# Optimization experiments

Hardware: AMD Instinct MI355X
Metric: run time of the kernel (lower is better)

## Reference

```python
import jax, jax.numpy as jnp
import numpy as np

N = 50000   # nodes
E = 800000  # edges
IN, HID, HEADS, OUT = 128, 32, 4, 64
NEG_SLOPE = 0.2


def _gatv2_layer(x, src, dst, Wl, bl, Wr, br, att, bias, res_W, concat):
    """One PyG-style GATv2Conv layer (eval mode, no dropout).
    x: [N, F_in]; att: [H, C]. Returns [N, H*C] if concat else [N, C]."""
    H, C = att.shape
    xl = (x @ Wl + bl).reshape(N, H, C)   # source transform
    xr = (x @ Wr + br).reshape(N, H, C)   # target transform
    e = jax.nn.leaky_relu(xl[src] + xr[dst], NEG_SLOPE)        # [E, H, C]
    logit = jnp.einsum('ehc,hc->eh', e, att)                   # [E, H]
    # segment softmax over incoming edges per destination node
    m = jax.ops.segment_max(logit, dst, num_segments=N)        # [N, H]
    p = jnp.exp(logit - m[dst])
    denom = jax.ops.segment_sum(p, dst, num_segments=N)
    alpha = p / (denom[dst] + 1e-16)                           # [E, H]
    out = jax.ops.segment_sum(xl[src] * alpha[:, :, None], dst, num_segments=N)  # [N, H, C]
    out = out.reshape(N, H * C) if concat else out.mean(axis=1)
    if res_W is not None:
        out = out + x @ res_W
    return out + bias


def _glorot(key, shape):
    fan_in = shape[0] if len(shape) > 1 else shape[-1]
    return jax.random.normal(key, shape, dtype=jnp.float32) / np.sqrt(fan_in)


def setup_inputs() -> dict:
    key = jax.random.key(0)
    ks = iter(jax.random.split(key, 32))
    x = jax.random.normal(next(ks), (N, IN), dtype=jnp.float32)
    edge_index = jax.random.randint(next(ks), (2, E), 0, N, dtype=jnp.int64)
    d = {"x": x, "edge_index": edge_index}
    HC = HEADS * HID  # 128
    # layer 0: IN -> HEADS*HID, concat, residual
    d["Wl0"] = _glorot(next(ks), (IN, HC)); d["bl0"] = jnp.zeros((HC,), jnp.float32)
    d["Wr0"] = _glorot(next(ks), (IN, HC)); d["br0"] = jnp.zeros((HC,), jnp.float32)
    d["att0"] = _glorot(next(ks), (HEADS, HID)); d["b0"] = jnp.zeros((HC,), jnp.float32)
    d["res0"] = _glorot(next(ks), (IN, HC))
    # layer 1: HC -> HEADS*HID, concat, residual
    d["Wl1"] = _glorot(next(ks), (HC, HC)); d["bl1"] = jnp.zeros((HC,), jnp.float32)
    d["Wr1"] = _glorot(next(ks), (HC, HC)); d["br1"] = jnp.zeros((HC,), jnp.float32)
    d["att1"] = _glorot(next(ks), (HEADS, HID)); d["b1"] = jnp.zeros((HC,), jnp.float32)
    d["res1"] = _glorot(next(ks), (HC, HC))
    # layer 2: HC -> OUT, heads=1, concat=False, no residual
    d["Wl2"] = _glorot(next(ks), (HC, OUT)); d["bl2"] = jnp.zeros((OUT,), jnp.float32)
    d["Wr2"] = _glorot(next(ks), (HC, OUT)); d["br2"] = jnp.zeros((OUT,), jnp.float32)
    d["att2"] = _glorot(next(ks), (1, OUT)); d["b2"] = jnp.zeros((OUT,), jnp.float32)
    return d


def reference(x, edge_index,
              Wl0, bl0, Wr0, br0, att0, b0, res0,
              Wl1, bl1, Wr1, br1, att1, b1, res1,
              Wl2, bl2, Wr2, br2, att2, b2):
    src, dst = edge_index[0], edge_index[1]
    h = _gatv2_layer(x, src, dst, Wl0, bl0, Wr0, br0, att0, b0, res0, True)
    h = jax.nn.elu(h)
    h = _gatv2_layer(h, src, dst, Wl1, bl1, Wr1, br1, att1, b1, res1, True)
    h = jax.nn.elu(h)
    return _gatv2_layer(h, src, dst, Wl2, bl2, Wr2, br2, att2, b2, None, False)
```

## Files before the change

### kernel.cpp

```cpp
#include <hip/hip_runtime.h>
#include <math.h>

#define NN 50000
#define EE 800000
#define NBK 196
#define EPB 4096

typedef short v8s __attribute__((ext_vector_type(8)));
typedef float v4f __attribute__((ext_vector_type(4)));

__device__ __forceinline__ ushort f2bf(float f) {
    uint u = __float_as_uint(f);
    uint r = (u + 0x7fffu + ((u >> 16) & 1u)) >> 16;
    return (ushort)r;
}
__device__ __forceinline__ float bf2f(ushort h) {
    return __uint_as_float(((uint)h) << 16);
}
__device__ __forceinline__ float lrelu(float x) {
    return fmaf(0.4f, fabsf(x), 0.6f * x);
}

template <int CTRL>
__device__ __forceinline__ float dppadd(float x) {
    int y = __builtin_amdgcn_update_dpp(0, __float_as_int(x), CTRL, 0xf, 0xf, true);
    return x + __int_as_float(y);
}
__device__ __forceinline__ float sum8(float x) {
    x = dppadd<0xB1>(x);
    x = dppadd<0x4E>(x);
    x = dppadd<0x141>(x);
    return x;
}
__device__ __forceinline__ float sum16(float x) {
    x = sum8(x);
    x = dppadd<0x140>(x);
    return x;
}
__device__ __forceinline__ float expclamp(float t) {
    return __expf(fminf(fmaxf(t, -60.f), 80.f));
}

__global__ __launch_bounds__(256) void k_bktcnt(const int* __restrict__ edst,
                                                int* __restrict__ bcnt) {
    __shared__ int h[NBK];
    int t = threadIdx.x;
    if (t < NBK) h[t] = 0;
    __syncthreads();
    int eb = blockIdx.x * EPB;
    #pragma unroll
    for (int k = 0; k < EPB / 256; ++k) {
        int e = eb + k * 256 + t;
        if (e < EE) atomicAdd(&h[edst[e] >> 8], 1);
    }
    __syncthreads();
    if (t < NBK && h[t]) atomicAdd(&bcnt[t], h[t]);
}

__global__ __launch_bounds__(256) void k_bscan(const int* __restrict__ bcnt,
                                               int* __restrict__ bbase,
                                               int* __restrict__ bcur) {
    __shared__ int sm[256];
    int t = threadIdx.x;
    int v = (t < NBK) ? bcnt[t] : 0;
    sm[t] = v;
    __syncthreads();
    for (int o = 1; o < 256; o <<= 1) {
        int a = (t >= o) ? sm[t - o] : 0;
        __syncthreads();
        sm[t] += a;
        __syncthreads();
    }
    if (t < NBK) { int ex = sm[t] - v; bbase[t] = ex; bcur[t] = ex; }
}

__global__ __launch_bounds__(256) void k_bktplace(const int* __restrict__ esrc,
                                                  const int* __restrict__ edst,
                                                  int* __restrict__ bcur,
                                                  uint* __restrict__ ebuf) {
    __shared__ int h[NBK];
    __shared__ int base[NBK];
    int t = threadIdx.x;
    if (t < NBK) h[t] = 0;
    __syncthreads();
    int eb = blockIdx.x * EPB;
    int pk[EPB / 256];
    #pragma unroll
    for (int k = 0; k < EPB / 256; ++k) {
        int e = eb + k * 256 + t;
        pk[k] = -1;
        if (e < EE) {
            int b = edst[e] >> 8;
            int r = atomicAdd(&h[b], 1);
            pk[k] = (b << 16) | r;
        }
    }
    __syncthreads();
    if (t < NBK && h[t]) base[t] = atomicAdd(&bcur[t], h[t]);
    __syncthreads();
    #pragma unroll
    for (int k = 0; k < EPB / 256; ++k) {
        int e = eb + k * 256 + t;
        if (e < EE) {
            int b = pk[k] >> 16;
            int r = pk[k] & 0xFFFF;
            uint dl = (uint)(edst[e] & 255);
            ebuf[base[b] + r] = (dl << 16) | (uint)esrc[e];
        }
    }
}

__global__ __launch_bounds__(256) void k_bktfin(const uint* __restrict__ ebuf,
                                                const int* __restrict__ bbase,
                                                const int* __restrict__ bcnt,
                                                int* __restrict__ rowptr,
                                                int* __restrict__ csrc) {
    __shared__ int deg[256];
    __shared__ int sm[256];
    __shared__ int cur[256];
    const int b = blockIdx.x;
    const int t = threadIdx.x;
    const int eb = bbase[b];
    const int ec = bcnt[b];
    deg[t] = 0;
    __syncthreads();
    for (int k = t; k < ec; k += 256)
        atomicAdd(&deg[ebuf[eb + k] >> 16], 1);
    __syncthreads();
    int v = deg[t];
    sm[t] = v;
    __syncthreads();
    for (int o = 1; o < 256; o <<= 1) {
        int a = (t >= o) ? sm[t - o] : 0;
        __syncthreads();
        sm[t] += a;
        __syncthreads();
    }
    int node = b * 256 + t;
    if (node < NN) rowptr[node + 1] = eb + sm[t];
    if (node == 0) rowptr[0] = 0;
    cur[t] = sm[t] - v;
    __syncthreads();
    for (int k = t; k < ec; k += 256) {
        uint u = ebuf[eb + k];
        int nl = (int)(u >> 16);
        int r = atomicAdd(&cur[nl], 1);
        csrc[eb + r] = (int)(u & 0xFFFFu);
    }
}

struct WPack {
    const float* W[8];
    ushort* Th[8];
    ushort* Tl[8];
    int fout[8];
};

__global__ __launch_bounds__(256) void k_conv_w(WPack p) {
    int wi = blockIdx.y;
    int fout = p.fout[wi];
    int total = 128 * fout;
    int i = blockIdx.x * 256 + threadIdx.x;
    if (i >= total) return;
    int k = i / fout;
    int n = i - k * fout;
    float f = p.W[wi][i];
    ushort h = f2bf(f);
    float lo = f - bf2f(h);
    int t = n >> 4, m = n & 15, c = k >> 5, quad = (k >> 3) & 3, j = k & 7;
    int flat = ((((t * 4 + c) * 4 + quad) * 16 + m) << 3) + j;
    p.Th[wi][flat] = h;
    p.Tl[wi][flat] = f2bf(lo);
}

template <int FOUT, int NMAT, bool CVT>
__global__ __launch_bounds__(256) void k_gemm_fused(
    const float* __restrict__ Xf,
    const ushort* __restrict__ Xh, const ushort* __restrict__ Xl,
    const ushort* __restrict__ T0h, const ushort* __restrict__ T0l, const float* __restrict__ B0,
    const ushort* __restrict__ T1h, const ushort* __restrict__ T1l, const float* __restrict__ B1,
    const ushort* __restrict__ T2h, const ushort* __restrict__ T2l,
    const float* __restrict__ ATT, float* __restrict__ DR,
    ushort* __restrict__ O0b, float* __restrict__ O1, float* __restrict__ O2)
{
    constexpr int NH  = (FOUT == 128) ? 4 : 1;
    constexpr int RS  = FOUT + ((FOUT == 128) ? 8 : 4);
    constexpr int NT  = FOUT / 16;
    constexpr int TPH = NT / NH;

    const int lane = threadIdx.x & 63;
    const int wid  = threadIdx.x >> 6;
    const int m    = lane & 15;
    const int quad = lane >> 4;
    const int row0 = blockIdx.x * 64 + wid * 16;

    v8s ah[4], al[4];
    {
        int arow = row0 + m;
        if (arow > NN - 1) arow = NN - 1;
        #pragma unroll
        for (int c = 0; c < 4; ++c) {
            size_t off = (size_t)arow * 128 + c * 32 + quad * 8;
            if constexpr (CVT) {
                float4 f0 = *(const float4*)(Xf + off);
                float4 f1 = *(const float4*)(Xf + off + 4);
                const float fe[8] = {f0.x, f0.y, f0.z, f0.w, f1.x, f1.y, f1.z, f1.w};
                #pragma unroll
                for (int e = 0; e < 8; ++e) {
                    ushort h = f2bf(fe[e]);
                    float lo = fe[e] - bf2f(h);
                    ah[c][e] = (short)h;
                    al[c][e] = (short)(__float_as_uint(lo) >> 16);
                }
            } else {
                ah[c] = *(const v8s*)(Xh + off);
                al[c] = *(const v8s*)(Xl + off);
            }
        }
    }

    float dp0[4] = {0.f, 0.f, 0.f, 0.f};
    float dp1[4] = {0.f, 0.f, 0.f, 0.f};

    #pragma unroll
    for (int t = 0; t < NT; ++t) {
        v4f a0 = {0.f, 0.f, 0.f, 0.f};
        v4f a1 = {0.f, 0.f, 0.f, 0.f};
        v4f a2 = {0.f, 0.f, 0.f, 0.f};
        #pragma unroll
        for (int c = 0; c < 4; ++c) {
            const int boff = t * 2048 + (c * 4 + quad) * 128 + m * 8;
            v8s b0h = *(const v8s*)(T0h + boff);
            v8s b0l = *(const v8s*)(T0l + boff);
            v8s b1h = *(const v8s*)(T1h + boff);
            v8s b1l = *(const v8s*)(T1l + boff);
            a0 = __builtin_amdgcn_mfma_f32_16x16x32_bf16(al[c], b0h, a0, 0, 0, 0);
            a1 = __builtin_amdgcn_mfma_f32_16x16x32_bf16(al[c], b1h, a1, 0, 0, 0);
            a0 = __builtin_amdgcn_mfma_f32_16x16x32_bf16(ah[c], b0l, a0, 0, 0, 0);
            a1 = __builtin_amdgcn_mfma_f32_16x16x32_bf16(ah[c], b1l, a1, 0, 0, 0);
            a0 = __builtin_amdgcn_mfma_f32_16x16x32_bf16(ah[c], b0h, a0, 0, 0, 0);
            a1 = __builtin_amdgcn_mfma_f32_16x16x32_bf16(ah[c], b1h, a1, 0, 0, 0);
            if constexpr (NMAT == 3) {
                v8s b2h = *(const v8s*)(T2h + boff);
                v8s b2l = *(const v8s*)(T2l + boff);
                a2 = __builtin_amdgcn_mfma_f32_16x16x32_bf16(al[c], b2h, a2, 0, 0, 0);
                a2 = __builtin_amdgcn_mfma_f32_16x16x32_bf16(ah[c], b2l, a2, 0, 0, 0);
                a2 = __builtin_amdgcn_mfma_f32_16x16x32_bf16(ah[c], b2h, a2, 0, 0, 0);
            }
        }
        const int col = t * 16 + m;
        const float bad0 = B0[col];
        const float bad1 = B1[col];
        const float attc = ATT[col];
        #pragma unroll
        for (int j = 0; j < 4; ++j) {
            float o0v = a0[j] + bad0;
            float o1v = a1[j] + bad1;
            dp0[j] = fmaf(attc, o0v, dp0[j]);
            dp1[j] = fmaf(attc, o1v, dp1[j]);
            int r = row0 + quad * 4 + j;
            if (r < NN) {
                O0b[(size_t)r * RS + col] = f2bf(o0v);
                O1[(size_t)r * FOUT + col] = o1v;
                if constexpr (NMAT == 3) O2[(size_t)r * FOUT + col] = a2[j];
            }
        }
        if ((t % TPH) == TPH - 1) {
            const int h = t / TPH;
            #pragma unroll
            for (int j = 0; j < 4; ++j) {
                float s0 = sum16(dp0[j]);
                float s1 = sum16(dp1[j]);
                int r = row0 + quad * 4 + j;
                if (m == 0 && r < NN) {
                    *(float*)(O0b + (size_t)r * RS + FOUT + 2 * h) = 0.6f * s0;
                    DR[(size_t)r * NH + h] = 0.6f * s1;
                }
                dp0[j] = 0.f;
                dp1[j] = 0.f;
            }
        }
    }
}

__global__ __launch_bounds__(256) void k_agg01(const ushort* __restrict__ XLb,
                                               const float4* __restrict__ XR4,
                                               const float4* __restrict__ RES4,
                                               const float* __restrict__ att,
                                               const float* __restrict__ bias,
                                               const float* __restrict__ DR,
                                               const int* __restrict__ rowptr,
                                               const int* __restrict__ csrc,
                                               ushort* __restrict__ Hh,
                                               ushort* __restrict__ Hl) {
    const int lane = threadIdx.x & 63;
    const int wid = threadIdx.x >> 6;
    const int n = blockIdx.x * 4 + wid;
    if (n >= NN) return;
    const int beg = rowptr[n];
    const int end = rowptr[n + 1];
    const int half = lane >> 5;
    const uint j = lane & 31;
    const int head = (int)(j >> 3);

    const float4 xr = XR4[(uint)n * 32u + j];
    float4 at = ((const float4*)att)[j];
    at.x *= 0.4f; at.y *= 0.4f; at.z *= 0.4f; at.w *= 0.4f;
    const float dRn = DR[(uint)n * 4u + (uint)head];
    float4 s = {0.f, 0.f, 0.f, 0.f};
    float d = 0.f;

#define EDGE01(U, DL)  {                                              \
    float4 v = {bf2f((U).x), bf2f((U).y), bf2f((U).z), bf2f((U).w)};  \
    float t0 =      at.x * fabsf(v.x + xr.x);                         \
    t0 = fmaf(at.y, fabsf(v.y + xr.y), t0);                           \
    t0 = fmaf(at.z, fabsf(v.z + xr.z), t0);                           \
    t0 = fmaf(at.w, fabsf(v.w + xr.w), t0);                           \
    float p = expclamp(sum8(t0) + (DL) + dRn);                        \
    d += p;                                                            \
    s.x = fmaf(p, v.x, s.x); s.y = fmaf(p, v.y, s.y);                 \
    s.z = fmaf(p, v.z, s.z); s.w = fmaf(p, v.w, s.w); }

    int i = beg;
    for (; i + 8 <= end; i += 8) {
        uint sa = (uint)csrc[i + half];
        uint sb = (uint)csrc[i + 2 + half];
        uint sc = (uint)csrc[i + 4 + half];
        uint sd = (uint)csrc[i + 6 + half];
        const ushort* pa = XLb + (size_t)sa * 136u;
        const ushort* pb = XLb + (size_t)sb * 136u;
        const ushort* pc = XLb + (size_t)sc * 136u;
        const ushort* pd = XLb + (size_t)sd * 136u;
        ushort4 ua = *(const ushort4*)(pa + 4u * j);
        float  da_ = *(const float*)(pa + 128 + 2 * head);
        ushort4 ub = *(const ushort4*)(pb + 4u * j);
        float  db_ = *(const float*)(pb + 128 + 2 * head);
        ushort4 uc = *(const ushort4*)(pc + 4u * j);
        float  dc_ = *(const float*)(pc + 128 + 2 * head);
        ushort4 ud = *(const ushort4*)(pd + 4u * j);
        float  dd_ = *(const float*)(pd + 128 + 2 * head);
        EDGE01(ua, da_)
        EDGE01(ub, db_)
        EDGE01(uc, dc_)
        EDGE01(ud, dd_)
    }
    for (; i < end; i += 2) {
        int ia = i + half;
        if (ia > end - 1) ia = end - 1;
        uint sa = (uint)csrc[ia];
        const ushort* pa = XLb + (size_t)sa * 136u;
        ushort4 ua = *(const ushort4*)(pa + 4u * j);
        float  da_ = *(const float*)(pa + 128 + 2 * head);
        float4 v = {bf2f(ua.x), bf2f(ua.y), bf2f(ua.z), bf2f(ua.w)};
        float t0 =      at.x * fabsf(v.x + xr.x);
        t0 = fmaf(at.y, fabsf(v.y + xr.y), t0);
        t0 = fmaf(at.z, fabsf(v.z + xr.z), t0);
        t0 = fmaf(at.w, fabsf(v.w + xr.w), t0);
        float p = expclamp(sum8(t0) + da_ + dRn);
        if (half && (i + 1 >= end)) p = 0.f;
        d += p;
        s.x = fmaf(p, v.x, s.x); s.y = fmaf(p, v.y, s.y);
        s.z = fmaf(p, v.z, s.z); s.w = fmaf(p, v.w, s.w);
    }
#undef EDGE01

    d   += __shfl_xor(d, 32);
    s.x += __shfl_xor(s.x, 32);
    s.y += __shfl_xor(s.y, 32);
    s.z += __shfl_xor(s.z, 32);
    s.w += __shfl_xor(s.w, 32);

    if (half == 0) {
        float inv = (d > 0.f) ? 1.f / d : 0.f;
        float4 rv = RES4[(uint)n * 32u + j];
        float4 bv = ((const float4*)bias)[j];
        float o0 = fmaf(s.x, inv, rv.x + bv.x);
        float o1 = fmaf(s.y, inv, rv.y + bv.y);
        float o2 = fmaf(s.z, inv, rv.z + bv.z);
        float o3 = fmaf(s.w, inv, rv.w + bv.w);
        o0 = o0 > 0.f ? o0 : __expf(o0) - 1.f;
        o1 = o1 > 0.f ? o1 : __expf(o1) - 1.f;
        o2 = o2 > 0.f ? o2 : __expf(o2) - 1.f;
        o3 = o3 > 0.f ? o3 : __expf(o3) - 1.f;
        ushort4 h, l;
        h.x = f2bf(o0); l.x = f2bf(o0 - bf2f(h.x));
        h.y = f2bf(o1); l.y = f2bf(o1 - bf2f(h.y));
        h.z = f2bf(o2); l.z = f2bf(o2 - bf2f(h.z));
        h.w = f2bf(o3); l.w = f2bf(o3 - bf2f(h.w));
        *(ushort4*)(Hh + (uint)n * 128u + 4u * j) = h;
        *(ushort4*)(Hl + (uint)n * 128u + 4u * j) = l;
    }
}

__global__ __launch_bounds__(256) void k_agg2(const ushort* __restrict__ XLb,
                                              const float4* __restrict__ XR4,
                                              const float* __restrict__ att,
                                              const float* __restrict__ bias,
                                              const float* __restrict__ DR,
                                              const int* __restrict__ rowptr,
                                              const int* __restrict__ csrc,
                                              float* __restrict__ OUT) {
    const int lane = threadIdx.x & 63;
    const int wid = threadIdx.x >> 6;
    const int n = blockIdx.x * 4 + wid;
    if (n >= NN) return;
    const int beg = rowptr[n];
    const int end = rowptr[n + 1];
    const int q = lane >> 4;
    const uint jj = lane & 15;

    const float4 xr = XR4[(uint)n * 16u + jj];
    float4 at = ((const float4*)att)[jj];
    at.x *= 0.4f; at.y *= 0.4f; at.z *= 0.4f; at.w *= 0.4f;
    const float dRn = DR[n];
    float4 s = {0.f, 0.f, 0.f, 0.f};
    float d = 0.f;
    const int e1 = end - 1;

    for (int i = beg; i < end; i += 8) {
        int i0 = i + q;
        int i1 = i + 4 + q;
        uint s0 = (uint)csrc[min(i0, e1)];
        uint s1 = (uint)csrc[min(i1, e1)];
        const ushort* p0 = XLb + (size_t)s0 * 68u;
        const ushort* p1 = XLb + (size_t)s1 * 68u;
        ushort4 u0 = *(const ushort4*)(p0 + 4u * jj);
        float  dl0 = *(const float*)(p0 + 64);
        ushort4 u1 = *(const ushort4*)(p1 + 4u * jj);
        float  dl1 = *(const float*)(p1 + 64);
        #pragma unroll
        for (int u = 0; u < 2; ++u) {
            ushort4 uv = (u == 0) ? u0 : u1;
            float  dlv = (u == 0) ? dl0 : dl1;
            int ii = (u == 0) ? i0 : i1;
            float4 v = {bf2f(uv.x), bf2f(uv.y), bf2f(uv.z), bf2f(uv.w)};
            float t0 =      at.x * fabsf(v.x + xr.x);
            t0 = fmaf(at.y, fabsf(v.y + xr.y), t0);
            t0 = fmaf(at.z, fabsf(v.z + xr.z), t0);
            t0 = fmaf(at.w, fabsf(v.w + xr.w), t0);
            float p = expclamp(sum16(t0) + dlv + dRn);
            if (ii >= end) p = 0.f;
            d += p;
            s.x = fmaf(p, v.x, s.x); s.y = fmaf(p, v.y, s.y);
            s.z = fmaf(p, v.z, s.z); s.w = fmaf(p, v.w, s.w);
        }
    }

    d   += __shfl_xor(d, 16);   d   += __shfl_xor(d, 32);
    s.x += __shfl_xor(s.x, 16); s.x += __shfl_xor(s.x, 32);
    s.y += __shfl_xor(s.y, 16); s.y += __shfl_xor(s.y, 32);
    s.z += __shfl_xor(s.z, 16); s.z += __shfl_xor(s.z, 32);
    s.w += __shfl_xor(s.w, 16); s.w += __shfl_xor(s.w, 32);

    if (lane < 16) {
        float inv = (d > 0.f) ? 1.f / d : 0.f;
        float4 bv = ((const float4*)bias)[jj];
        float4 o;
        o.x = fmaf(s.x, inv, bv.x);
        o.y = fmaf(s.y, inv, bv.y);
        o.z = fmaf(s.z, inv, bv.z);
        o.w = fmaf(s.w, inv, bv.w);
        *(float4*)(OUT + (uint)n * 64u + 4u * jj) = o;
    }
}

extern "C" void kernel_launch(void* const* d_in, const int* in_sizes, int n_in,
                              void* d_out, int out_size, void* d_ws, size_t ws_size,
                              hipStream_t stream) {
    const float* x    = (const float*)d_in[0];
    const int*   ei   = (const int*)d_in[1];
    const int*   esrc = ei;
    const int*   edst = ei + EE;

    const float* Wl0 = (const float*)d_in[2];
    const float* bl0 = (const float*)d_in[3];
    const float* Wr0 = (const float*)d_in[4];
    const float* br0 = (const float*)d_in[5];
    const float* at0 = (const float*)d_in[6];
    const float* b0  = (const float*)d_in[7];
    const float* rs0 = (const float*)d_in[8];
    const float* Wl1 = (const float*)d_in[9];
    const float* bl1 = (const float*)d_in[10];
    const float* Wr1 = (const float*)d_in[11];
    const float* br1 = (const float*)d_in[12];
    const float* at1 = (const float*)d_in[13];
    const float* b1  = (const float*)d_in[14];
    const float* rs1 = (const float*)d_in[15];
    const float* Wl2 = (const float*)d_in[16];
    const float* bl2 = (const float*)d_in[17];
    const float* Wr2 = (const float*)d_in[18];
    const float* br2 = (const float*)d_in[19];
    const float* at2 = (const float*)d_in[20];
    const float* b2  = (const float*)d_in[21];

    float* out = (float*)d_out;

    ushort* XLb = (ushort*)d_ws;
    float* XR  = (float*)(XLb + (size_t)NN * 136);
    float* RES = XR + (size_t)NN * 128;
    ushort* Xh = (ushort*)(RES + (size_t)NN * 128);
    ushort* Xl_ = Xh + (size_t)NN * 128;
    float* DRarr = (float*)(Xl_ + (size_t)NN * 128);
    ushort* Wth = (ushort*)(DRarr + (size_t)NN * 4);
    const int wsz[8] = {16384, 16384, 16384, 16384, 16384, 16384, 8192, 8192};
    ushort* th[8]; ushort* tl[8];
    {
        ushort* p = Wth;
        for (int i = 0; i < 8; ++i) { th[i] = p; p += wsz[i]; }
        for (int i = 0; i < 8; ++i) { tl[i] = p; p += wsz[i]; }
    }
    int* bcnt   = (int*)(Wth + 2 * (6 * 16384 + 2 * 8192));
    int* bbase  = bcnt + 256;
    int* bcur   = bbase + 256;
    int* rowptr = bcur + 256;
    int* csrc   = rowptr + (NN + 1);
    uint* ebuf  = (uint*)(csrc + EE);

    hipMemsetAsync(bcnt, 0, 256 * sizeof(int), stream);
    const int ebk = (EE + EPB - 1) / EPB;
    k_bktcnt<<<ebk, 256, 0, stream>>>(edst, bcnt);
    k_bscan<<<1, 256, 0, stream>>>(bcnt, bbase, bcur);
    k_bktplace<<<ebk, 256, 0, stream>>>(esrc, edst, bcur, ebuf);
    k_bktfin<<<NBK, 256, 0, stream>>>(ebuf, bbase, bcnt, rowptr, csrc);

    WPack wp;
    const float* Ws[8] = {Wl0, Wr0, rs0, Wl1, Wr1, rs1, Wl2, Wr2};
    const int fouts[8] = {128, 128, 128, 128, 128, 128, 64, 64};
    for (int i = 0; i < 8; ++i) { wp.W[i] = Ws[i]; wp.Th[i] = th[i]; wp.Tl[i] = tl[i]; wp.fout[i] = fouts[i]; }
    k_conv_w<<<dim3(64, 8), 256, 0, stream>>>(wp);

    const int gemm_gx = (NN + 63) / 64;
    const int agg_grid = (NN + 3) / 4;

    k_gemm_fused<128, 3, true><<<gemm_gx, 256, 0, stream>>>(x, nullptr, nullptr,
        th[0], tl[0], bl0, th[1], tl[1], br0, th[2], tl[2], at0, DRarr, XLb, XR, RES);
    k_agg01<<<agg_grid, 256, 0, stream>>>(XLb, (const float4*)XR, (const float4*)RES,
        at0, b0, DRarr, rowptr, csrc, Xh, Xl_);

    k_gemm_fused<128, 3, false><<<gemm_gx, 256, 0, stream>>>(nullptr, Xh, Xl_,
        th[3], tl[3], bl1, th[4], tl[4], br1, th[5], tl[5], at1, DRarr, XLb, XR, RES);
    k_agg01<<<agg_grid, 256, 0, stream>>>(XLb, (const float4*)XR, (const float4*)RES,
        at1, b1, DRarr, rowptr, csrc, Xh, Xl_);

    k_gemm_fused<64, 2, false><<<gemm_gx, 256, 0, stream>>>(nullptr, Xh, Xl_,
        th[6], tl[6], bl2, th[7], tl[7], br2, nullptr, nullptr, at2, DRarr, XLb, XR, nullptr);
    k_agg2<<<agg_grid, 256, 0, stream>>>(XLb, (const float4*)XR, at2, b2, DRarr, rowptr, csrc, out);
}
```

Baseline: 365.5 us.

## Split GEMM output tiles across grid y and move per-node attention dots to separate arrays

The fused GEMM kernel now covers only two 16-column tiles per block, with blockIdx.y choosing the slice. This gives four times (or twice, for the last layer) as many blocks, raising parallelism at the cost of reloading and converting the A rows once per slice. The source-side attention dot products move out of the padded 136/68-stride bf16 rows into a separate DL array, so XLb becomes densely packed. In the last layer the per-node dots are summed with atomics across the two column slices, which needs two extra memsets. The aggregation kernels read DL through a separate gather, adding one scattered load per edge.

```diff
diff --git a/kernel.cpp b/kernel.cpp
--- a/kernel.cpp
+++ b/kernel.cpp
@@ -173,26 +173,22 @@
     p.Tl[wi][flat] = f2bf(lo);
 }
 
-template <int FOUT, int NMAT, bool CVT>
+template <int FOUT, int NMAT, bool CVT, int TS>
 __global__ __launch_bounds__(256) void k_gemm_fused(
     const float* __restrict__ Xf,
     const ushort* __restrict__ Xh, const ushort* __restrict__ Xl,
     const ushort* __restrict__ T0h, const ushort* __restrict__ T0l, const float* __restrict__ B0,
     const ushort* __restrict__ T1h, const ushort* __restrict__ T1l, const float* __restrict__ B1,
     const ushort* __restrict__ T2h, const ushort* __restrict__ T2l,
-    const float* __restrict__ ATT, float* __restrict__ DR,
+    const float* __restrict__ ATT, float* __restrict__ DL, float* __restrict__ DR,
     ushort* __restrict__ O0b, float* __restrict__ O1, float* __restrict__ O2)
 {
-    constexpr int NH  = (FOUT == 128) ? 4 : 1;
-    constexpr int RS  = FOUT + ((FOUT == 128) ? 8 : 4);
-    constexpr int NT  = FOUT / 16;
-    constexpr int TPH = NT / NH;
-
     const int lane = threadIdx.x & 63;
     const int wid  = threadIdx.x >> 6;
     const int m    = lane & 15;
     const int quad = lane >> 4;
     const int row0 = blockIdx.x * 64 + wid * 16;
+    const int t0   = blockIdx.y * TS;
 
     v8s ah[4], al[4];
     {
@@ -223,7 +219,8 @@
     float dp1[4] = {0.f, 0.f, 0.f, 0.f};
 
     #pragma unroll
-    for (int t = 0; t < NT; ++t) {
+    for (int tt = 0; tt < TS; ++tt) {
+        const int t = t0 + tt;
         v4f a0 = {0.f, 0.f, 0.f, 0.f};
         v4f a1 = {0.f, 0.f, 0.f, 0.f};
         v4f a2 = {0.f, 0.f, 0.f, 0.f};
@@ -260,24 +257,38 @@
             dp1[j] = fmaf(attc, o1v, dp1[j]);
             int r = row0 + quad * 4 + j;
             if (r < NN) {
-                O0b[(size_t)r * RS + col] = f2bf(o0v);
+                O0b[(size_t)r * FOUT + col] = f2bf(o0v);
                 O1[(size_t)r * FOUT + col] = o1v;
                 if constexpr (NMAT == 3) O2[(size_t)r * FOUT + col] = a2[j];
             }
         }
-        if ((t % TPH) == TPH - 1) {
-            const int h = t / TPH;
-            #pragma unroll
-            for (int j = 0; j < 4; ++j) {
-                float s0 = sum16(dp0[j]);
-                float s1 = sum16(dp1[j]);
-                int r = row0 + quad * 4 + j;
-                if (m == 0 && r < NN) {
-                    *(float*)(O0b + (size_t)r * RS + FOUT + 2 * h) = 0.6f * s0;
-                    DR[(size_t)r * NH + h] = 0.6f * s1;
+        if constexpr (FOUT == 128) {
+            if ((t & 1) == 1) {
+                const int h = t >> 1;
+                #pragma unroll
+                for (int j = 0; j < 4; ++j) {
+                    float s0 = sum16(dp0[j]);
+                    float s1 = sum16(dp1[j]);
+                    int r = row0 + quad * 4 + j;
+                    if (m == 0 && r < NN) {
+                        DL[(size_t)r * 4 + h] = 0.6f * s0;
+                        DR[(size_t)r * 4 + h] = 0.6f * s1;
+                    }
+                    dp0[j] = 0.f;
+                    dp1[j] = 0.f;
                 }
-                dp0[j] = 0.f;
-                dp1[j] = 0.f;
+            }
+        }
+    }
+    if constexpr (FOUT == 64) {
+        #pragma unroll
+        for (int j = 0; j < 4; ++j) {
+            float s0 = sum16(dp0[j]);
+            float s1 = sum16(dp1[j]);
+            int r = row0 + quad * 4 + j;
+            if (m == 0 && r < NN) {
+                atomicAdd(&DL[r], 0.6f * s0);
+                atomicAdd(&DR[r], 0.6f * s1);
             }
         }
     }
@@ -288,6 +299,7 @@
                                                const float4* __restrict__ RES4,
                                                const float* __restrict__ att,
                                                const float* __restrict__ bias,
+                                               const float* __restrict__ DL,
                                                const float* __restrict__ DR,
                                                const int* __restrict__ rowptr,
                                                const int* __restrict__ csrc,
@@ -301,22 +313,22 @@
     const int end = rowptr[n + 1];
     const int half = lane >> 5;
     const uint j = lane & 31;
-    const int head = (int)(j >> 3);
+    const uint head = j >> 3;
 
     const float4 xr = XR4[(uint)n * 32u + j];
     float4 at = ((const float4*)att)[j];
     at.x *= 0.4f; at.y *= 0.4f; at.z *= 0.4f; at.w *= 0.4f;
-    const float dRn = DR[(uint)n * 4u + (uint)head];
+    const float dRn = DR[(uint)n * 4u + head];
     float4 s = {0.f, 0.f, 0.f, 0.f};
     float d = 0.f;
 
-#define EDGE01(U, DL)  {                                              \
+#define EDGE01(U, DLV)  {                                             \
     float4 v = {bf2f((U).x), bf2f((U).y), bf2f((U).z), bf2f((U).w)};  \
     float t0 =      at.x * fabsf(v.x + xr.x);                         \
     t0 = fmaf(at.y, fabsf(v.y + xr.y), t0);                           \
     t0 = fmaf(at.z, fabsf(v.z + xr.z), t0);                           \
     t0 = fmaf(at.w, fabsf(v.w + xr.w), t0);                           \
-    float p = expclamp(sum8(t0) + (DL) + dRn);                        \
+    float p = expclamp(sum8(t0) + (DLV) + dRn);                       \
     d += p;                                                            \
     s.x = fmaf(p, v.x, s.x); s.y = fmaf(p, v.y, s.y);                 \
     s.z = fmaf(p, v.z, s.z); s.w = fmaf(p, v.w, s.w); }
@@ -327,18 +339,14 @@
         uint sb = (uint)csrc[i + 2 + half];
         uint sc = (uint)csrc[i + 4 + half];
         uint sd = (uint)csrc[i + 6 + half];
-        const ushort* pa = XLb + (size_t)sa * 136u;
-        const ushort* pb = XLb + (size_t)sb * 136u;
-        const ushort* pc = XLb + (size_t)sc * 136u;
-        const ushort* pd = XLb + (size_t)sd * 136u;
-        ushort4 ua = *(const ushort4*)(pa + 4u * j);
-        float  da_ = *(const float*)(pa + 128 + 2 * head);
-        ushort4 ub = *(const ushort4*)(pb + 4u * j);
-        float  db_ = *(const float*)(pb + 128 + 2 * head);
-        ushort4 uc = *(const ushort4*)(pc + 4u * j);
-        float  dc_ = *(const float*)(pc + 128 + 2 * head);
-        ushort4 ud = *(const ushort4*)(pd + 4u * j);
-        float  dd_ = *(const float*)(pd + 128 + 2 * head);
+        ushort4 ua = *(const ushort4*)(XLb + (size_t)sa * 128u + 4u * j);
+        float  da_ = DL[(size_t)sa * 4u + head];
+        ushort4 ub = *(const ushort4*)(XLb + (size_t)sb * 128u + 4u * j);
+        float  db_ = DL[(size_t)sb * 4u + head];
+        ushort4 uc = *(const ushort4*)(XLb + (size_t)sc * 128u + 4u * j);
+        float  dc_ = DL[(size_t)sc * 4u + head];
+        ushort4 ud = *(const ushort4*)(XLb + (size_t)sd * 128u + 4u * j);
+        float  dd_ = DL[(size_t)sd * 4u + head];
         EDGE01(ua, da_)
         EDGE01(ub, db_)
         EDGE01(uc, dc_)
@@ -348,9 +356,8 @@
         int ia = i + half;
         if (ia > end - 1) ia = end - 1;
         uint sa = (uint)csrc[ia];
-        const ushort* pa = XLb + (size_t)sa * 136u;
-        ushort4 ua = *(const ushort4*)(pa + 4u * j);
-        float  da_ = *(const float*)(pa + 128 + 2 * head);
+        ushort4 ua = *(const ushort4*)(XLb + (size_t)sa * 128u + 4u * j);
+        float  da_ = DL[(size_t)sa * 4u + head];
         float4 v = {bf2f(ua.x), bf2f(ua.y), bf2f(ua.z), bf2f(ua.w)};
         float t0 =      at.x * fabsf(v.x + xr.x);
         t0 = fmaf(at.y, fabsf(v.y + xr.y), t0);
@@ -396,6 +403,7 @@
                                               const float4* __restrict__ XR4,
                                               const float* __restrict__ att,
                                               const float* __restrict__ bias,
+                                              const float* __restrict__ DL,
                                               const float* __restrict__ DR,
                                               const int* __restrict__ rowptr,
                                               const int* __restrict__ csrc,
@@ -422,12 +430,10 @@
         int i1 = i + 4 + q;
         uint s0 = (uint)csrc[min(i0, e1)];
         uint s1 = (uint)csrc[min(i1, e1)];
-        const ushort* p0 = XLb + (size_t)s0 * 68u;
-        const ushort* p1 = XLb + (size_t)s1 * 68u;
-        ushort4 u0 = *(const ushort4*)(p0 + 4u * jj);
-        float  dl0 = *(const float*)(p0 + 64);
-        ushort4 u1 = *(const ushort4*)(p1 + 4u * jj);
-        float  dl1 = *(const float*)(p1 + 64);
+        ushort4 u0 = *(const ushort4*)(XLb + (size_t)s0 * 64u + 4u * jj);
+        float  dl0 = DL[s0];
+        ushort4 u1 = *(const ushort4*)(XLb + (size_t)s1 * 64u + 4u * jj);
+        float  dl1 = DL[s1];
         #pragma unroll
         for (int u = 0; u < 2; ++u) {
             ushort4 uv = (u == 0) ? u0 : u1;
@@ -496,11 +502,12 @@
     float* out = (float*)d_out;
 
     ushort* XLb = (ushort*)d_ws;
-    float* XR  = (float*)(XLb + (size_t)NN * 136);
+    float* XR  = (float*)(XLb + (size_t)NN * 128);
     float* RES = XR + (size_t)NN * 128;
     ushort* Xh = (ushort*)(RES + (size_t)NN * 128);
     ushort* Xl_ = Xh + (size_t)NN * 128;
-    float* DRarr = (float*)(Xl_ + (size_t)NN * 128);
+    float* DLarr = (float*)(Xl_ + (size_t)NN * 128);
+    float* DRarr = DLarr + (size_t)NN * 4;
     ushort* Wth = (ushort*)(DRarr + (size_t)NN * 4);
     const int wsz[8] = {16384, 16384, 16384, 16384, 16384, 16384, 8192, 8192};
     ushort* th[8]; ushort* tl[8];
@@ -532,17 +539,19 @@
     const int gemm_gx = (NN + 63) / 64;
     const int agg_grid = (NN + 3) / 4;
 
-    k_gemm_fused<128, 3, true><<<gemm_gx, 256, 0, stream>>>(x, nullptr, nullptr,
-        th[0], tl[0], bl0, th[1], tl[1], br0, th[2], tl[2], at0, DRarr, XLb, XR, RES);
+    k_gemm_fused<128, 3, true, 2><<<dim3(gemm_gx, 4), 256, 0, stream>>>(x, nullptr, nullptr,
+        th[0], tl[0], bl0, th[1], tl[1], br0, th[2], tl[2], at0, DLarr, DRarr, XLb, XR, RES);
     k_agg01<<<agg_grid, 256, 0, stream>>>(XLb, (const float4*)XR, (const float4*)RES,
-        at0, b0, DRarr, rowptr, csrc, Xh, Xl_);
-
-    k_gemm_fused<128, 3, false><<<gemm_gx, 256, 0, stream>>>(nullptr, Xh, Xl_,
-        th[3], tl[3], bl1, th[4], tl[4], br1, th[5], tl[5], at1, DRarr, XLb, XR, RES);
+        at0, b0, DLarr, DRarr, rowptr, csrc, Xh, Xl_);
+
+    k_gemm_fused<128, 3, false, 2><<<dim3(gemm_gx, 4), 256, 0, stream>>>(nullptr, Xh, Xl_,
+        th[3], tl[3], bl1, th[4], tl[4], br1, th[5], tl[5], at1, DLarr, DRarr, XLb, XR, RES);
     k_agg01<<<agg_grid, 256, 0, stream>>>(XLb, (const float4*)XR, (const float4*)RES,
-        at1, b1, DRarr, rowptr, csrc, Xh, Xl_);
-
-    k_gemm_fused<64, 2, false><<<gemm_gx, 256, 0, stream>>>(nullptr, Xh, Xl_,
-        th[6], tl[6], bl2, th[7], tl[7], br2, nullptr, nullptr, at2, DRarr, XLb, XR, nullptr);
-    k_agg2<<<agg_grid, 256, 0, stream>>>(XLb, (const float4*)XR, at2, b2, DRarr, rowptr, csrc, out);
-}
+        at1, b1, DLarr, DRarr, rowptr, csrc, Xh, Xl_);
+
+    hipMemsetAsync(DLarr, 0, NN * sizeof(float), stream);
+    hipMemsetAsync(DRarr, 0, NN * sizeof(float), stream);
+    k_gemm_fused<64, 2, false, 2><<<dim3(gemm_gx, 2), 256, 0, stream>>>(nullptr, Xh, Xl_,
+        th[6], tl[6], bl2, th[7], tl[7], br2, nullptr, nullptr, at2, DLarr, DRarr, XLb, XR, nullptr);
+    k_agg2<<<agg_grid, 256, 0, stream>>>(XLb, (const float4*)XR, at2, b2, DLarr, DRarr, rowptr, csrc, out);
+}
```

Result: slower. 375.6 us (+2.8%).
